# Optimization experiments

Hardware: AMD Instinct MI355X
Metric: run time of the kernel (lower is better)

The kernel has to match this reference:

```python
import jax, jax.numpy as jnp
import numpy as np

BSZ, SL, K, D_IN, D_OUT = 2, 1024, 24, 512, 512
K_U, K_Y = 3, 2
USE_HANKEL_L = False


def get_top_eigh(l, k, use_hankel_L):
    i = np.arange(1, l + 1, dtype=np.float64)
    s = i[:, None] + i[None, :]
    if use_hankel_L:
        Z = ((-1.0) ** (s - 2.0) + 1.0) * 8.0 / ((s + 3.0) * (s - 1.0) * (s + 1.0))
    else:
        Z = 2.0 / (s ** 3 - s)
    sigma, phi = np.linalg.eigh(Z)  # ascending
    return jnp.asarray(sigma[-k:], jnp.float32), jnp.asarray(phi[:, -k:], jnp.float32)


def shift(x, k):
    # causal shift along time axis 1, zero-padded at the front
    if k == 0:
        return x
    return jnp.pad(x, ((0, 0), (k, 0), (0, 0)))[:, : x.shape[1]]


def fft_causal_conv(filters, u):
    # filters: (l, k); u: (b, l, d) -> (b, l, k, d) causal convolution per filter
    l = u.shape[1]
    n = 2 * l
    F = jnp.fft.rfft(filters, n=n, axis=0)  # (n//2+1, k)
    U = jnp.fft.rfft(u, n=n, axis=1)        # (b, n//2+1, d)
    Y = jnp.fft.irfft(U[:, :, None, :] * F[None, :, :, None], n=n, axis=1)
    return Y[:, :l].astype(u.dtype)


def compute_ar_u(M_u, u):
    # ar_u[b,t,o] = sum_{i<k_u} M_u[i] @ u_{t-i}
    U = jnp.stack([shift(u, i) for i in range(M_u.shape[0])])  # (k_u, b, l, d_in)
    return jnp.einsum('koi,kbli->blo', M_u, U)


def compute_spectral(u, sigma, phi, M_phi_plus, M_phi_minus, m_y):
    l = u.shape[1]
    phi_s = phi * sigma ** 0.25  # eigenvalue-scaled spectral filters (l, k)
    U_plus = fft_causal_conv(phi_s, u)  # (b, l, k, d_in)
    spec = jnp.einsum('blki,koi->blo', U_plus, M_phi_plus)
    if not USE_HANKEL_L:
        # negative-featurization branch: filters modulated by (-1)^i
        alt = ((-1.0) ** jnp.arange(l)).astype(u.dtype)
        U_minus = fft_causal_conv(phi_s * alt[:, None], u)
        spec = spec + jnp.einsum('blki,koi->blo', U_minus, M_phi_minus)
    if m_y is not None:
        spec = shift(spec, m_y.shape[0])  # spectral features enter at lag k_y (paper: t-2)
    return spec


def compute_ar_y(m_y, y):
    # true short linear recurrence on outputs:
    # yhat_t = y_t + sum_{i=1}^{k_y} m_y[i-1] @ yhat_{t-i}; returns the correction term
    k_y, d_out = m_y.shape[0], m_y.shape[1]
    b = y.shape[0]

    def step(carry, y_t):  # carry: (k_y, b, d_out) = [yhat_{t-1}, ..., yhat_{t-k_y}]
        ar_t = jnp.einsum('koj,kbj->bo', m_y, carry)
        yhat_t = y_t + ar_t
        carry = jnp.concatenate([yhat_t[None], carry[:-1]], axis=0)
        return carry, ar_t

    y_tl = jnp.swapaxes(y, 0, 1)  # (l, b, d_out)
    _, ar = jax.lax.scan(step, jnp.zeros((k_y, b, d_out), y.dtype), y_tl)
    return jnp.swapaxes(ar, 0, 1)


def setup_inputs() -> dict:
    key = jax.random.key(0)
    k0, k1, k2, k3, k4 = jax.random.split(key, 5)
    inputs = jax.random.normal(k0, (BSZ, SL, D_IN), jnp.float32)
    M_u = jax.random.normal(k1, (K_U, D_OUT, D_IN), jnp.float32) * 0.02
    M_phi_plus = jax.random.normal(k2, (K, D_OUT, D_IN), jnp.float32) * 0.02
    M_phi_minus = jax.random.normal(k3, (K, D_OUT, D_IN), jnp.float32) * 0.02
    m_y = jax.random.normal(k4, (K_Y, D_OUT, D_OUT), jnp.float32) * 0.02
    sigma, phi = get_top_eigh(SL, K, USE_HANKEL_L)
    return {'inputs': inputs, 'M_u': M_u, 'M_phi_plus': M_phi_plus,
            'M_phi_minus': M_phi_minus, 'm_y': m_y, 'sigma': sigma, 'phi': phi}


def reference(inputs, M_u, M_phi_plus, M_phi_minus, m_y, sigma, phi):
    ar_u = compute_ar_u(M_u, inputs)
    spectral = compute_spectral(inputs, sigma, phi, M_phi_plus, M_phi_minus, m_y)
    y_t = ar_u + spectral
    y_t = y_t + compute_ar_y(m_y, y_t)  # learnable_m_y=True branch
    return y_t  # dropout p=0.0 (identity)
```

## Files before the change

### kernel.cpp

```cpp
#include <hip/hip_runtime.h>
#include <hip/hip_bf16.h>


typedef unsigned short u16;
typedef __attribute__((ext_vector_type(8))) short  vshort8;
typedef __attribute__((ext_vector_type(4))) short  vshort4;
typedef __attribute__((ext_vector_type(4))) float  f32x4;
typedef __attribute__((ext_vector_type(4))) unsigned int vuint4;

__device__ __forceinline__ u16 f2b(float x) {
  __hip_bfloat16 h = __float2bfloat16(x);
  return __builtin_bit_cast(u16, h);
}
__device__ __forceinline__ float b2f(u16 x) {
  unsigned int u = ((unsigned int)x) << 16;
  return __builtin_bit_cast(float, u);
}

__device__ __forceinline__ void gll16(const u16* g, u16* l) {
  __builtin_amdgcn_global_load_lds((__attribute__((address_space(1))) void*)g,
                                   (__attribute__((address_space(3))) void*)l,
                                   16, 0, 0);
}

#define A2T_B  25165824
#define A2T_CJ 3145728
#define A2T_KH 65536

struct GB {
  const u16* A; const u16* B;
  float* Cf; u16* Cb;
  const float* zf; float* out;
  u16* A2T; u16* Au;
  const u16* zp;
  int M, N;
};

template<int V>
__global__ __launch_bounds__(V == 0 ? 512 : 256) void g2(GB a) {
  const int tid = threadIdx.x;
  int bn = blockIdx.x, bm = blockIdx.y;
  int zz = blockIdx.z;
  int cj = 0, cb = 0, cd = 0, slot = 0;
  int kbeg = 0, kend = 0;
  if (V == 0) {
    int f = blockIdx.x;
    int o = (f & 7) * 204 + (f >> 3);
    bm = o & 15; bn = o >> 4; kend = 512;
  }
  if (V == 1) {
    int f = blockIdx.x;
    int o = (f & 7) * 144 + (f >> 3);
    const int offs1[8] = {0, 256, 480, 672, 832, 960, 1056, 1120};
    cj = 0;
    if (o >= offs1[1]) cj = 1;
    if (o >= offs1[2]) cj = 2;
    if (o >= offs1[3]) cj = 3;
    if (o >= offs1[4]) cj = 4;
    if (o >= offs1[5]) cj = 5;
    if (o >= offs1[6]) cj = 6;
    if (o >= offs1[7]) cj = 7;
    int r = o - offs1[cj];
    int run = 8 - cj;
    int combo = r / run;
    bm = cj + (r - combo * run);
    int zzc = combo >> 2; bn = combo & 3;
    cb = zzc & 1; cd = bm - cj;
    slot = zzc * 8 + cj;
    kbeg = (zzc >> 1) * 1536; kend = kbeg + 1536;
  }
  if (V == 2) {
    int f = blockIdx.x;
    int o = (f & 7) * 68 + (f >> 3);
    const int offs2[16] = {0, 64, 124, 180, 232, 280, 324, 364,
                           400, 432, 460, 484, 504, 520, 532, 540};
    int s = 0;
#pragma unroll
    for (int c = 1; c < 16; ++c)
      if (o >= offs2[c]) s = c;
    int r = o - offs2[s];
    bm = s + (r >> 2); bn = r & 3;
    zz = s;
    kbeg = s * 1024; kend = kbeg + 1024;
  }
  const int m0 = bm * 128;
  const int n0 = (V == 0) ? bn * 256 : bn * 128;
  if (V == 3 || V == 5 || V == 6 || V == 7) kend = 1024;

  __shared__ u16 smem[V == 0 ? 24576 : 16384];
  f32x4 acc[4][4];
#pragma unroll
  for (int i = 0; i < 4; i++)
#pragma unroll
    for (int j = 0; j < 4; j++) acc[i][j] = f32x4{0.f, 0.f, 0.f, 0.f};

  const int lane = tid & 63, wv = tid >> 6;
  const int wr = (V == 0) ? (wv >> 2) : (wv >> 1);
  const int wc = (V == 0) ? (wv & 3) : (wv & 1);
  const u16* Ap = a.A;
  if (V == 5) Ap = a.A + (size_t)zz * 524288;
  const u16* zpl = a.zp + lane * 8;

  auto gaddrA = [&](int it, int k0) -> const u16* {
    int lrow = (it * 4 + wv) * 16 + (lane & 15);
    int kk = k0 + ((lane >> 4) << 3);
    if (V == 1) return Ap + (size_t)cd * 786432 + (size_t)lrow * 6144 + kk;
    if (V == 2) {
      int m = m0 + lrow, j = m >> 6, b = (m >> 5) & 1, c = m & 31;
      int tau = kk >> 9, p = kk & 511;
      if (tau > j) return zpl;
      return Ap + (size_t)(b * 1024 + c * 32 + j - tau) * 512 + p;
    }
    if (V == 3) { int m = m0 + lrow; return (m < a.M) ? Ap + (size_t)m * 1024 + kk : zpl; }
    if (V == 5) return Ap + (size_t)(m0 + lrow) * 1024 + kk;
    if (V == 6) return (lrow < 64) ? Ap + (size_t)lrow * 1024 + kk : zpl;
    if (lrow < 32) {
      int b = lrow & 1, k2 = lrow >> 1;
      return Ap + (size_t)(b * 32 + 2 * k2) * 1024 + kk;
    }
    return zpl;
  };
  auto gaddrB = [&](int it, int k0) -> const u16* {
    int lrow = (it * 4 + wv) * 16 + (lane & 15);
    int kk = k0 + ((lane >> 4) << 3);
    int n = n0 + lrow;
    if (V == 1) {
      int kh = kk >> 7, sp = kk & 127;
      return a.B + (size_t)cb * A2T_B + (size_t)cj * A2T_CJ
           + (size_t)kh * A2T_KH + (size_t)n * 128 + sp;
    }
    if (V == 2) {
      int tau = kk >> 9, p = kk & 511;
      return a.B + (size_t)tau * 524288 + (size_t)n * 1024 + p;
    }
    if (V == 3) {
      int jn = n >> 9, o = n & 511;
      return a.B + (size_t)(jn + 1) * 524288 + (size_t)o * 1024 + kk;
    }
    if (V == 5) return a.B + (size_t)n * 1024 + kk;
    return (n < 512)
        ? a.B + (size_t)32 * 524288 + (size_t)n * 1024 + kk
        : a.B + (size_t)31 * 524288 + (size_t)(n - 512) * 1024 + kk;
  };

  auto stage = [&](int c, int k0) {
    if (V == 0) {
      int kk = k0 + ((lane >> 4) << 3);
      int lrowA = wv * 16 + (lane & 15);
      gll16(Ap + (size_t)(m0 + lrowA) * 512 + kk, smem + c * 4096 + wv * 512);
#pragma unroll
      for (int it = 0; it < 2; ++it) {
        int lrowB = (it * 8 + wv) * 16 + (lane & 15);
        gll16(a.B + (size_t)(n0 + lrowB) * 512 + kk,
              smem + 8192 + c * 8192 + (it * 8 + wv) * 512);
      }
    } else {
#pragma unroll
      for (int it = 0; it < 2; ++it) {
        int weff = wv + it * 4;
        gll16(gaddrA(it, k0), smem + c * 4096 + weff * 512);
        gll16(gaddrB(it, k0), smem + 8192 + c * 4096 + weff * 512);
      }
    }
  };

  if (kbeg < kend) stage(0, kbeg);
  __syncthreads();
  int cur = 0;
  for (int k0 = kbeg; k0 < kend; k0 += 32) {
    if (k0 + 32 < kend) stage(cur ^ 1, k0 + 32);
    vshort8 af[4], bf_[4];
#pragma unroll
    for (int s = 0; s < 4; s++) {
      af[s] = *(const vshort8*)&smem[cur * 4096 +
                (((wr * 4 + s) * 4 + (lane >> 4)) * 16 + (lane & 15)) * 8];
      if (V == 0)
        bf_[s] = *(const vshort8*)&smem[8192 + cur * 8192 +
                  (((wc * 4 + s) * 4 + (lane >> 4)) * 16 + (lane & 15)) * 8];
      else
        bf_[s] = *(const vshort8*)&smem[8192 + cur * 4096 +
                  (((wc * 4 + s) * 4 + (lane >> 4)) * 16 + (lane & 15)) * 8];
    }
#pragma unroll
    for (int i = 0; i < 4; i++)
#pragma unroll
      for (int j = 0; j < 4; j++)
        acc[i][j] = __builtin_amdgcn_mfma_f32_16x16x32_bf16(af[i], bf_[j], acc[i][j], 0, 0, 0);
    __syncthreads();
    cur ^= 1;
  }

  if (V == 0 && bn < 96) {
    const int strd = 136;
    const int b = m0 >> 10;
    const int cjw = (m0 & 1023) >> 7;
#pragma unroll
    for (int p = 0; p < 4; ++p) {
      __syncthreads();
      if (wc == p) {
#pragma unroll
        for (int i = 0; i < 4; i++) {
#pragma unroll
          for (int j = 0; j < 4; j++) {
            f32x4 v = acc[i][j];
            int mloc = wr * 64 + i * 16 + ((lane >> 4) << 2);
            int phys = j * 16 + (lane & 15);
            vshort4 pk = { (short)f2b(v[0]), (short)f2b(v[1]),
                           (short)f2b(v[2]), (short)f2b(v[3]) };
            *(vshort4*)&smem[phys * strd + mloc] = pk;
          }
        }
      }
      __syncthreads();
      int rowp = tid >> 3, t8 = tid & 7;
      int n = n0 + p * 64 + rowp;
      int o = n & 511, kh = n >> 9;
      u16* dst = a.A2T + (size_t)b * A2T_B + (size_t)cjw * A2T_CJ
               + (size_t)kh * A2T_KH + (size_t)o * 128 + t8 * 16;
      const u16* srcl = &smem[rowp * strd + t8 * 16];
      *(vuint4*)(dst)     = *(const vuint4*)(srcl);
      *(vuint4*)(dst + 8) = *(const vuint4*)(srcl + 8);
    }
    return;
  }

#pragma unroll
  for (int i = 0; i < 4; i++) {
    int em = m0 + wr * 64 + i * 16 + ((lane >> 4) << 2);
#pragma unroll
    for (int j = 0; j < 4; j++) {
      int n = n0 + wc * 64 + j * 16 + (lane & 15);
      f32x4 v = acc[i][j];
      if (V == 0) {
        int b = em >> 10, s = em & 1023;
        int jj = (n - 24576) >> 9, o = n & 511;
#pragma unroll
        for (int t = 0; t < 4; t++)
          a.Au[((size_t)(b * 3 + jj) * 1024 + (s + t)) * 512 + o] = f2b(v[t]);
      } else if (V == 1) {
        u16* C = a.Cb + (size_t)slot * 524288;
#pragma unroll
        for (int t = 0; t < 4; t++) C[(size_t)(em + t) * 512 + n] = f2b(v[t]);
      } else if (V == 2) {
        float* C = a.Cf + (size_t)zz * 1048576;
#pragma unroll
        for (int t = 0; t < 4; t++) C[(size_t)(em + t) * 512 + n] = v[t];
      } else if (V == 3) {
        int jj = n >> 9, oo = n & 511;
#pragma unroll
        for (int t = 0; t < 4; t++) {
          int m = em + t;
          if (m < a.M) {
            int b = m >> 5, c = m & 31;
            float zv = a.zf[(size_t)(jj * 64 + b * 32 + c) * 512 + oo];
            a.out[(size_t)b * 524288 + (size_t)(c * 32 + jj) * 512 + oo] = v[t] + zv;
          }
        }
      } else if (V == 5) {
        u16* C = a.Cb + (size_t)zz * 524288;
#pragma unroll
        for (int t = 0; t < 4; t++) C[(size_t)(em + t) * 1024 + n] = f2b(v[t]);
      } else if (V == 6) {
        int jrow = (n < 512) ? 31 : 30, oo = n & 511;
#pragma unroll
        for (int t = 0; t < 4; t++) {
          int m = em + t;
          if (m < 62) {
            int b = m & 1, c = m >> 1;
            a.Cf[(size_t)m * 1024 + n] =
                v[t] + a.zf[(size_t)(jrow * 64 + b * 32 + (c + 1)) * 512 + oo];
          }
        }
      } else {
        int jrow = (n < 512) ? 31 : 30, oo = n & 511;
#pragma unroll
        for (int t = 0; t < 4; t++) {
          int m = em + t;
          if (m < 32) {
            int b = m & 1, k2 = m >> 1;
            float val = v[t] + a.zf[(size_t)(jrow * 64 + b * 32 + 2 * k2) * 512 + oo];
            a.Cb[(size_t)(b * 32 + 2 * k2 + 1) * 1024 + n] = f2b(val);
          }
        }
      }
    }
  }
}

__global__ void k_prep_phis(const float* __restrict__ phi, const float* __restrict__ sigma,
                            float* __restrict__ phis) {
  int i = blockIdx.x * 256 + threadIdx.x;
  if (i >= 1024 * 48) return;
  int tau = i / 48, kf = i % 48, k = (kf >= 24) ? kf - 24 : kf;
  float v = phi[tau * 24 + k] * powf(sigma[k], 0.25f);
  if (kf >= 24 && (tau & 1)) v = -v;
  phis[i] = v;
}

__global__ void k_prep_all(const float* __restrict__ u, const float* __restrict__ Mp,
                           const float* __restrict__ Mm, const float* __restrict__ Mu,
                           const float* __restrict__ phis,
                           u16* __restrict__ X, u16* __restrict__ W1,
                           u16* __restrict__ Wtoep) {
  int gid = blockIdx.x * 256 + threadIdx.x;
  if (gid < 262144) {
    int i4 = gid * 4;
    f32x4 v = *(const f32x4*)(u + i4);
    vshort4 pk = { (short)f2b(v[0]), (short)f2b(v[1]), (short)f2b(v[2]), (short)f2b(v[3]) };
    *(vshort4*)(X + i4) = pk;
  }
#pragma unroll
  for (int r = 0; r < 4; ++r) {
    int item = gid + r * 1048576;
    if (item < 3342336) {
      int i4 = item * 4;
      const float* src; int off;
      if (i4 < 6291456) { src = Mp; off = i4; }
      else if (i4 < 12582912) { src = Mm; off = i4 - 6291456; }
      else { src = Mu; off = i4 - 12582912; }
      f32x4 v = *(const f32x4*)(src + off);
      vshort4 pk = { (short)f2b(v[0]), (short)f2b(v[1]), (short)f2b(v[2]), (short)f2b(v[3]) };
      *(vshort4*)(W1 + i4) = pk;
    }
  }
  if (gid < 786432) {
    int i = gid * 8;
    int kap = i % 6144, row = i / 6144;
    int tp = row & 127, d = row >> 7;
    int kh = kap >> 7, sp = kap & 127;
    int tau0 = d * 128 + tp - sp;
    u16 vals[8];
#pragma unroll
    for (int e = 0; e < 8; ++e) {
      int tau = tau0 - e;
      vals[e] = (tau >= 0 && tau < 1024) ? f2b(phis[tau * 48 + kh]) : (u16)0;
    }
    *(vuint4*)(Wtoep + i) = *(const vuint4*)vals;
  }
}

__global__ void k_initTop(const float* __restrict__ my, u16* __restrict__ Top) {
  int i = blockIdx.x * 256 + threadIdx.x;
  if (i >= 1048576) return;
  int mat = i >> 19, rem = i & 524287, o = rem >> 10, k = rem & 1023;
  u16 v;
  if (mat == 0) v = (k == o) ? (u16)0x3F80 : (u16)0;
  else v = (k < 512) ? f2b(my[o * 512 + k]) : f2b(my[262144 + o * 512 + (k - 512)]);
  Top[i] = v;
}

__global__ __launch_bounds__(256) void k_transT(const u16* __restrict__ Top,
                                                u16* __restrict__ STc, int c) {
  __shared__ u16 tile[64][72];
  int tx = blockIdx.x, ty = blockIdx.y;
  int tid = threadIdx.x;
  int r = tid >> 2, seg = tid & 3;
  int k = ty * 64 + r;
  const u16* src = (k < 512) ? Top + (size_t)c * 524288 + (size_t)k * 1024 + tx * 64
                             : Top + (size_t)(c - 1) * 524288 + (size_t)(k - 512) * 1024 + tx * 64;
  *(vuint4*)&tile[r][seg * 16]     = *(const vuint4*)(src + seg * 16);
  *(vuint4*)&tile[r][seg * 16 + 8] = *(const vuint4*)(src + seg * 16 + 8);
  __syncthreads();
  int n = tx * 64 + r;
  u16 tmp[16];
#pragma unroll
  for (int j = 0; j < 16; j++) tmp[j] = tile[seg * 16 + j][r];
  *(vuint4*)&STc[(size_t)n * 1024 + ty * 64 + seg * 16]     = *(vuint4*)&tmp[0];
  *(vuint4*)&STc[(size_t)n * 1024 + ty * 64 + seg * 16 + 8] = *(vuint4*)&tmp[8];
}

__device__ __forceinline__ void addp(float* acc, vuint4 v) {
  const unsigned int* vu = (const unsigned int*)&v;
#pragma unroll
  for (int e = 0; e < 4; ++e) {
    unsigned int pw = vu[e];
    acc[2 * e]     += __builtin_bit_cast(float, (pw & 0xffffu) << 16);
    acc[2 * e + 1] += __builtin_bit_cast(float, pw & 0xffff0000u);
  }
}

__global__ void k_combine(const u16* __restrict__ parts, const u16* __restrict__ Au,
                          u16* __restrict__ ybf) {
  int i = blockIdx.x * 256 + threadIdx.x;
  if (i >= 131072) return;
  int og = i & 63, t = (i >> 6) & 1023, b = i >> 16;
  float acc[8];
#pragma unroll
  for (int e = 0; e < 8; ++e) acc[e] = 0.f;
#pragma unroll
  for (int j = 0; j < 3; j++)
    if (t >= j)
      addp(acc, *(const vuint4*)(Au + ((size_t)(b * 3 + j) * 1024 + (t - j)) * 512 + og * 8));
  if (t >= 2) {
    int tp = t - 2, bmv = tp >> 7;
#pragma unroll
    for (int g = 0; g < 8; ++g) {
      if ((g & 1) != b) continue;
      const u16* base = parts + (size_t)(g * 8) * 524288 + (size_t)tp * 512 + og * 8;
      for (int j = 0; j <= bmv; ++j)
        addp(acc, *(const vuint4*)(base + (size_t)j * 524288));
    }
  }
  u16 o16[8];
#pragma unroll
  for (int e = 0; e < 8; ++e) o16[e] = f2b(acc[e]);
  *(vuint4*)(ybf + ((size_t)(b * 1024 + t)) * 512 + og * 8) = *(vuint4*)o16;
}

__global__ void k_zred(const float* __restrict__ zp, float* __restrict__ z,
                       u16* __restrict__ Wm, float* __restrict__ bnd,
                       u16* __restrict__ Abnd) {
  int i = blockIdx.x * 256 + threadIdx.x;
  if (i < 2048) bnd[i] = 0.f;
  if (i < 1024) { Abnd[i] = 0; Abnd[32768 + i] = 0; }
  if (i >= 1048576) return;
  int nsum = (i >> 16) + 1;
  float s = 0.f;
  for (int j = 0; j < nsum; ++j) s += zp[(size_t)j * 1048576 + i];
  z[i] = s;
  int m = i >> 9, jj = m >> 6, rem = m & 63, b = rem >> 5, c = rem & 31, oo = i & 511;
  if (jj == 31) Wm[(size_t)((c << 1) | b) * 1024 + oo] = f2b(s);
  if (jj == 30) Wm[(size_t)((c << 1) | b) * 1024 + 512 + oo] = f2b(s);
}

__global__ __launch_bounds__(256) void k_bnd2(const u16* __restrict__ Top,
                                              const float* __restrict__ ubuf,
                                              float* __restrict__ bnd,
                                              u16* __restrict__ Abnd, int k) {
  __shared__ float st[2048];
  int tid = threadIdx.x;
  const float* s0 = bnd + (size_t)k * 2048;
  for (int j = tid; j < 2048; j += 256) st[j] = s0[j];
  __syncthreads();
  int q4 = blockIdx.x * 256 + tid;
  int q = q4 >> 2, quarter = q4 & 3;
  int b = q >> 10, kk = q & 1023;
  const u16* row = (kk < 512) ? Top + (size_t)64 * 524288 + (size_t)kk * 1024
                              : Top + (size_t)63 * 524288 + (size_t)(kk - 512) * 1024;
  const float* stb = st + b * 1024 + quarter * 256;
  const u16* rp = row + quarter * 256;
  float sum = 0.f;
  for (int t = 0; t < 32; ++t) {
    vuint4 v = *(const vuint4*)(rp + t * 8);
    const unsigned int* vu = (const unsigned int*)&v;
#pragma unroll
    for (int e = 0; e < 4; ++e) {
      unsigned int pw = vu[e];
      float lo = __builtin_bit_cast(float, (pw & 0xffffu) << 16);
      float hi = __builtin_bit_cast(float, pw & 0xffff0000u);
      sum += lo * stb[t * 8 + e * 2] + hi * stb[t * 8 + e * 2 + 1];
    }
  }
  sum += __shfl_xor(sum, 1);
  sum += __shfl_xor(sum, 2);
  if (quarter == 0) {
    float s = sum + ubuf[(size_t)(4 * k + b) * 1024 + kk];
    bnd[(size_t)(k + 1) * 2048 + b * 1024 + kk] = s;
    Abnd[(size_t)(b * 32 + 2 * k + 2) * 1024 + kk] = f2b(s);
  }
}

extern "C" void kernel_launch(void* const* d_in, const int* in_sizes, int n_in,
                              void* d_out, int out_size, void* d_ws, size_t ws_size,
                              hipStream_t stream) {
  const float* u     = (const float*)d_in[0];
  const float* Mu    = (const float*)d_in[1];
  const float* Mp    = (const float*)d_in[2];
  const float* Mm    = (const float*)d_in[3];
  const float* my    = (const float*)d_in[4];
  const float* sigma = (const float*)d_in[5];
  const float* phi   = (const float*)d_in[6];
  float* out = (float*)d_out;

  char* ws = (char*)d_ws;
  size_t off = 0;
  auto alc = [&](size_t b) { size_t p = off; off = (off + b + 255) & ~(size_t)255; return p; };
  u16*  X     = (u16*)(ws + alc(2097152));
  u16*  Wtoep = (u16*)(ws + alc(12582912));
  u16*  A2T   = (u16*)(ws + alc(100663296));
  u16*  Au    = (u16*)(ws + alc(6291456));
  u16*  W1    = (u16*)(ws + alc(26738688));
  char* ptail = ws + alc(40370176); (void)ptail;
  float* phis = (float*)(ws + alc(196608));
  float* bnd  = (float*)(ws + alc(131072));
  u16*  Abnd  = (u16*)(ws + alc(131072));
  u16*  Wm    = (u16*)(ws + alc(131072));
  float* ubuf = (float*)(ws + alc(262144));
  u16*  zpad  = (u16*)(ws + alc(32768));
  if (off > ws_size) return;
  u16*  partsBf = (u16*)W1;
  float* zparts = (float*)W1;
  u16*  ybf = A2T;
  float* zf = (float*)((char*)A2T + (4 << 20));
  u16*  Top = (u16*)((char*)A2T + (size_t)(8 << 20));
  u16*  STc = (u16*)((char*)A2T + (size_t)(76 << 20));

  hipMemsetAsync(zpad, 0, 32768, stream);

  k_prep_phis<<<dim3(192), 256, 0, stream>>>(phi, sigma, phis);
  k_prep_all<<<dim3(4096), 256, 0, stream>>>(u, Mp, Mm, Mu, phis, X, W1, Wtoep);

  {
    GB g{}; g.A = X; g.B = W1; g.A2T = A2T; g.Au = Au; g.zp = zpad;
    g.M = 2048; g.N = 26112;
    g2<0><<<dim3(1632), 512, 0, stream>>>(g);
  }
  {
    GB g{}; g.A = Wtoep; g.B = A2T; g.Cb = partsBf; g.zp = zpad;
    g.M = 1024; g.N = 512;
    g2<1><<<dim3(1152), 256, 0, stream>>>(g);
  }
  k_combine<<<dim3(512), 256, 0, stream>>>(partsBf, Au, ybf);

  k_initTop<<<dim3(4096), 256, 0, stream>>>(my, Top);
  {
    const int cs[5] = {1, 2, 4, 8, 16};
    for (int li = 0; li < 5; ++li) {
      int c = cs[li];
      k_transT<<<dim3(16, 16), 256, 0, stream>>>(Top, STc, c);
      GB s{}; s.A = Top + 524288; s.B = STc; s.Cb = Top + (size_t)(c + 1) * 524288;
      s.zp = zpad; s.M = 512; s.N = 1024;
      g2<5><<<dim3(8, 4, c), 256, 0, stream>>>(s);
    }
    k_transT<<<dim3(16, 16), 256, 0, stream>>>(Top, STc, 32);
    GB s{}; s.A = Top + (size_t)31 * 524288; s.B = STc;
    s.Cb = Top + (size_t)63 * 524288; s.zp = zpad; s.M = 512; s.N = 1024;
    g2<5><<<dim3(8, 4, 2), 256, 0, stream>>>(s);
  }

  {
    GB g{}; g.A = ybf; g.B = Top; g.Cf = zparts; g.zp = zpad;
    g.M = 2048; g.N = 512;
    g2<2><<<dim3(544), 256, 0, stream>>>(g);
  }
  k_zred<<<dim3(4096), 256, 0, stream>>>(zparts, zf, Wm, bnd, Abnd);

  {
    GB g{}; g.A = Wm; g.B = Top; g.Cf = ubuf; g.zf = zf; g.zp = zpad;
    g.M = 64; g.N = 1024;
    g2<6><<<dim3(8, 1, 1), 256, 0, stream>>>(g);
  }
  for (int k = 0; k < 15; ++k)
    k_bnd2<<<dim3(32), 256, 0, stream>>>(Top, ubuf, bnd, Abnd, k);
  {
    GB g{}; g.A = Abnd; g.B = Top; g.Cb = Abnd; g.zf = zf; g.zp = zpad;
    g.M = 32; g.N = 1024;
    g2<7><<<dim3(8, 1, 1), 256, 0, stream>>>(g);
  }

  {
    GB g{}; g.A = Abnd; g.B = Top; g.zf = zf; g.out = out; g.zp = zpad;
    g.M = 64; g.N = 16384;
    g2<3><<<dim3(128, 1, 1), 256, 0, stream>>>(g);
  }
}
```

Baseline: 700.0 us.

## Emit transposed bf16 power matrices from GEMM epilogue instead of separate transpose kernels

The doubling-GEMM chain that builds powers of the recurrence companion matrix used to launch a transpose kernel before every step to make the B operand. Now each V=5 GEMM also writes a transposed copy of its output tile through shared memory into a separate buffer P, and only for the blocks whose results later steps need. k_initTop seeds P with transposed identity and m_y blocks. This removes six transpose launches and their global traffic, at the cost of an extra LDS-staged store in the epilogue. It also moves the last step's output from slot 63 to slot 33, and k_bnd2 reads accordingly.

```diff
diff --git a/kernel.cpp b/kernel.cpp
--- a/kernel.cpp
+++ b/kernel.cpp
@@ -33,6 +33,7 @@
   const float* zf; float* out;
   u16* A2T; u16* Au;
   const u16* zp;
+  u16* Pb; int cidx; int pthr;
   int M, N;
 };
 
@@ -137,7 +138,11 @@
       int jn = n >> 9, o = n & 511;
       return a.B + (size_t)(jn + 1) * 524288 + (size_t)o * 1024 + kk;
     }
-    if (V == 5) return a.B + (size_t)n * 1024 + kk;
+    if (V == 5) {
+      return (kk < 512)
+          ? a.Pb + (size_t)a.cidx * 524288 + (size_t)n * 512 + kk
+          : a.Pb + (size_t)(a.cidx - 1) * 524288 + (size_t)n * 512 + (kk - 512);
+    }
     return (n < 512)
         ? a.B + (size_t)32 * 524288 + (size_t)n * 1024 + kk
         : a.B + (size_t)31 * 524288 + (size_t)(n - 512) * 1024 + kk;
@@ -285,6 +290,38 @@
       }
     }
   }
+
+  if (V == 5) {
+    if (zz >= a.pthr) {
+      const int strd = 136;
+      u16* Pout = a.Pb + (size_t)(a.cidx + 1 + zz) * 524288;
+#pragma unroll
+      for (int p = 0; p < 2; ++p) {
+        __syncthreads();
+        if (wc == p) {
+#pragma unroll
+          for (int i = 0; i < 4; i++) {
+#pragma unroll
+            for (int j = 0; j < 4; j++) {
+              f32x4 v = acc[i][j];
+              int mloc = wr * 64 + i * 16 + ((lane >> 4) << 2);
+              int phys = j * 16 + (lane & 15);
+              vshort4 pk = { (short)f2b(v[0]), (short)f2b(v[1]),
+                             (short)f2b(v[2]), (short)f2b(v[3]) };
+              *(vshort4*)&smem[phys * strd + mloc] = pk;
+            }
+          }
+        }
+        __syncthreads();
+        int rowp = tid >> 2, t4 = tid & 3;
+        u16* dst = Pout + (size_t)(n0 + p * 64 + rowp) * 512 + m0 + t4 * 32;
+        const u16* srcl = &smem[rowp * strd + t4 * 32];
+#pragma unroll
+        for (int q = 0; q < 4; ++q)
+          *(vuint4*)(dst + q * 8) = *(const vuint4*)(srcl + q * 8);
+      }
+    }
+  }
 }
 
 __global__ void k_prep_phis(const float* __restrict__ phi, const float* __restrict__ sigma,
@@ -339,34 +376,24 @@
   }
 }
 
-__global__ void k_initTop(const float* __restrict__ my, u16* __restrict__ Top) {
+__global__ void k_initTop(const float* __restrict__ my, u16* __restrict__ Top,
+                          u16* __restrict__ P) {
   int i = blockIdx.x * 256 + threadIdx.x;
-  if (i >= 1048576) return;
-  int mat = i >> 19, rem = i & 524287, o = rem >> 10, k = rem & 1023;
-  u16 v;
-  if (mat == 0) v = (k == o) ? (u16)0x3F80 : (u16)0;
-  else v = (k < 512) ? f2b(my[o * 512 + k]) : f2b(my[262144 + o * 512 + (k - 512)]);
-  Top[i] = v;
-}
-
-__global__ __launch_bounds__(256) void k_transT(const u16* __restrict__ Top,
-                                                u16* __restrict__ STc, int c) {
-  __shared__ u16 tile[64][72];
-  int tx = blockIdx.x, ty = blockIdx.y;
-  int tid = threadIdx.x;
-  int r = tid >> 2, seg = tid & 3;
-  int k = ty * 64 + r;
-  const u16* src = (k < 512) ? Top + (size_t)c * 524288 + (size_t)k * 1024 + tx * 64
-                             : Top + (size_t)(c - 1) * 524288 + (size_t)(k - 512) * 1024 + tx * 64;
-  *(vuint4*)&tile[r][seg * 16]     = *(const vuint4*)(src + seg * 16);
-  *(vuint4*)&tile[r][seg * 16 + 8] = *(const vuint4*)(src + seg * 16 + 8);
-  __syncthreads();
-  int n = tx * 64 + r;
-  u16 tmp[16];
-#pragma unroll
-  for (int j = 0; j < 16; j++) tmp[j] = tile[seg * 16 + j][r];
-  *(vuint4*)&STc[(size_t)n * 1024 + ty * 64 + seg * 16]     = *(vuint4*)&tmp[0];
-  *(vuint4*)&STc[(size_t)n * 1024 + ty * 64 + seg * 16 + 8] = *(vuint4*)&tmp[8];
+  if (i >= 2097152) return;
+  if (i < 1048576) {
+    int mat = i >> 19, rem = i & 524287, o = rem >> 10, k = rem & 1023;
+    u16 v;
+    if (mat == 0) v = (k == o) ? (u16)0x3F80 : (u16)0;
+    else v = (k < 512) ? f2b(my[o * 512 + k]) : f2b(my[262144 + o * 512 + (k - 512)]);
+    Top[i] = v;
+  } else {
+    int j = i - 1048576;
+    int mat = j >> 19, rem = j & 524287, n = rem >> 9, m = rem & 511;
+    u16 v;
+    if (mat == 0) v = (n == m) ? (u16)0x3F80 : (u16)0;
+    else v = (n < 512) ? f2b(my[m * 512 + n]) : f2b(my[262144 + m * 512 + (n - 512)]);
+    P[(size_t)mat * 524288 + (size_t)n * 512 + m] = v;
+  }
 }
 
 __device__ __forceinline__ void addp(float* acc, vuint4 v) {
@@ -435,8 +462,8 @@
   int q4 = blockIdx.x * 256 + tid;
   int q = q4 >> 2, quarter = q4 & 3;
   int b = q >> 10, kk = q & 1023;
-  const u16* row = (kk < 512) ? Top + (size_t)64 * 524288 + (size_t)kk * 1024
-                              : Top + (size_t)63 * 524288 + (size_t)(kk - 512) * 1024;
+  const u16* row = (kk < 512) ? Top + (size_t)34 * 524288 + (size_t)kk * 1024
+                              : Top + (size_t)33 * 524288 + (size_t)(kk - 512) * 1024;
   const float* stb = st + b * 1024 + quarter * 256;
   const u16* rp = row + quarter * 256;
   float sum = 0.f;
@@ -493,7 +520,7 @@
   u16*  ybf = A2T;
   float* zf = (float*)((char*)A2T + (4 << 20));
   u16*  Top = (u16*)((char*)A2T + (size_t)(8 << 20));
-  u16*  STc = (u16*)((char*)A2T + (size_t)(76 << 20));
+  u16*  P   = (u16*)((char*)A2T + (size_t)(44 << 20));
 
   hipMemsetAsync(zpad, 0, 32768, stream);
 
@@ -512,19 +539,20 @@
   }
   k_combine<<<dim3(512), 256, 0, stream>>>(partsBf, Au, ybf);
 
-  k_initTop<<<dim3(4096), 256, 0, stream>>>(my, Top);
+  k_initTop<<<dim3(8192), 256, 0, stream>>>(my, Top, P);
   {
     const int cs[5] = {1, 2, 4, 8, 16};
     for (int li = 0; li < 5; ++li) {
       int c = cs[li];
-      k_transT<<<dim3(16, 16), 256, 0, stream>>>(Top, STc, c);
-      GB s{}; s.A = Top + 524288; s.B = STc; s.Cb = Top + (size_t)(c + 1) * 524288;
+      GB s{}; s.A = Top + 524288; s.Cb = Top + (size_t)(c + 1) * 524288;
+      s.Pb = P; s.cidx = c; s.pthr = c - 2;
       s.zp = zpad; s.M = 512; s.N = 1024;
       g2<5><<<dim3(8, 4, c), 256, 0, stream>>>(s);
     }
-    k_transT<<<dim3(16, 16), 256, 0, stream>>>(Top, STc, 32);
-    GB s{}; s.A = Top + (size_t)31 * 524288; s.B = STc;
-    s.Cb = Top + (size_t)63 * 524288; s.zp = zpad; s.M = 512; s.N = 1024;
+    GB s{}; s.A = Top + (size_t)31 * 524288;
+    s.Cb = Top + (size_t)33 * 524288;
+    s.Pb = P; s.cidx = 32; s.pthr = 99;
+    s.zp = zpad; s.M = 512; s.N = 1024;
     g2<5><<<dim3(8, 4, 2), 256, 0, stream>>>(s);
   }
 
```

After: 692.9 us, median of 2. Within noise of the previous version (-1.0%).
